# Kernel tuning notes

Measured on AMD Instinct MI355X. Metric: run time of the kernel, lower is better.

Reference implementation:

```python
import jax, jax.numpy as jnp
import numpy as np

C = 32          # mid_channel / in_channel
B = 8           # batch size (number of scenes)
N = 2_000_000   # total points across batch
BN_EPS = 1e-4   # BatchNorm1d eps from norm_fn


def setup_inputs() -> dict:
    key = jax.random.key(0)
    ks = jax.random.split(key, 8)
    s = 0.05
    return {
        "feats": jax.random.normal(ks[0], (N, C), dtype=jnp.float32),
        "batch_idxs": jnp.sort(jax.random.randint(ks[1], (N,), 0, B, dtype=jnp.int32)),
        "off_w1": jax.random.normal(ks[2], (C, C), dtype=jnp.float32) * s,
        "off_b1": jnp.zeros((C,), jnp.float32),
        "bn_gamma": jnp.ones((C,), jnp.float32),   # set_bn_init fills 1.0
        "bn_beta": jnp.zeros((C,), jnp.float32),   # set_bn_init fills 0.0
        "off_w2": jax.random.normal(ks[3], (C, 3), dtype=jnp.float32) * s,
        "off_b2": jnp.zeros((3,), jnp.float32),
        "mask_w1": jax.random.normal(ks[4], (C, C), dtype=jnp.float32) * s,
        "mask_b1": jnp.zeros((C,), jnp.float32),
        "mask_w2": jax.random.normal(ks[5], (C, 1), dtype=jnp.float32) * s,
        "mask_b2": jnp.zeros((1,), jnp.float32),
        "iou_w": jax.random.normal(ks[6], (C, 1), dtype=jnp.float32) * s,
        "iou_b": jnp.zeros((1,), jnp.float32),
    }


def reference(feats, batch_idxs, off_w1, off_b1, bn_gamma, bn_beta, off_w2, off_b2,
              mask_w1, mask_b1, mask_w2, mask_b2, iou_w, iou_b):
    # offset_linear = MLP([C, C, 3], norm_fn=BatchNorm1d): Linear -> BN -> ReLU -> Linear
    h = feats @ off_w1 + off_b1                      # [N, C]
    mu = h.mean(axis=0)
    var = jnp.mean(jnp.square(h - mu), axis=0)       # biased var (torch BN training fwd)
    h = (h - mu) * jax.lax.rsqrt(var + BN_EPS) * bn_gamma + bn_beta
    h = jax.nn.relu(h)
    pt_offsets = h @ off_w2 + off_b2                 # [N, 3]

    # mask_linear = MLP([C, C, 1], norm_fn=None): Linear -> ReLU -> Linear
    m = jax.nn.relu(feats @ mask_w1 + mask_b1)       # [N, C]
    mask_scores = m @ mask_w2 + mask_b2              # [N, 1]

    # global_pool: scatter mean of features over per-batch segments (batch offsets)
    ones = jnp.ones((feats.shape[0],), feats.dtype)
    counts = jax.ops.segment_sum(ones, batch_idxs, num_segments=B)          # [B]
    pooled = jax.ops.segment_sum(feats, batch_idxs, num_segments=B)         # [B, C]
    pooled = pooled / jnp.maximum(counts, 1.0)[:, None]

    # iou_score_linear on the pooled proposal feature
    iou_scores = pooled @ iou_w + iou_b              # [B, 1]
    return pt_offsets, mask_scores, pooled, iou_scores
```

## Files before the change

kernel.cpp:

```cpp
#include <hip/hip_runtime.h>

#define TPB 256

typedef __attribute__((ext_vector_type(8))) short short8;
typedef __attribute__((ext_vector_type(4))) float floatx4;

__device__ __forceinline__ unsigned short bf_trunc(float f){
    union { float f; unsigned u; } c; c.f = f;
    return (unsigned short)(c.u >> 16);
}
__device__ __forceinline__ unsigned short bf_rne(float f){
    union { float f; unsigned u; } c; c.f = f;
    unsigned r = c.u + 0x7fffu + ((c.u >> 16) & 1u);
    return (unsigned short)(r >> 16);
}

__global__ __launch_bounds__(TPB, 4) void pass1_kernel(
    const float* __restrict__ feats, const int* __restrict__ bidx,
    const float* __restrict__ w1, const float* __restrict__ b1,
    const float* __restrict__ mw1, const float* __restrict__ mb1,
    const float* __restrict__ mw2, const float* __restrict__ mb2,
    float* __restrict__ mask_out,
    float* __restrict__ ws_sum, float* __restrict__ ws_sq,
    float* __restrict__ ws_pool, int N)
{
    __shared__ float s_pool[8][32];
    __shared__ float s_sum[32];
    __shared__ float s_sq[32];

    const int tid  = threadIdx.x;
    const int lane = tid & 63;
    const int p = lane & 15;
    const int q = lane >> 4;

    if (tid < 32){ s_sum[tid] = 0.f; s_sq[tid] = 0.f; }
    ((float*)s_pool)[tid] = 0.f;
    __syncthreads();

    short8 aw0, aw1, am0, am1;
    floatx4 ci_h0, ci_h1, ci_m0, ci_m1;
    float mw2v[8];
#pragma unroll
    for (int j = 0; j < 8; ++j){
        const int k = q * 8 + j;
        aw0[j] = (short)bf_rne(w1 [k * 32 + p]);
        aw1[j] = (short)bf_rne(w1 [k * 32 + 16 + p]);
        am0[j] = (short)bf_rne(mw1[k * 32 + p]);
        am1[j] = (short)bf_rne(mw1[k * 32 + 16 + p]);
    }
#pragma unroll
    for (int r = 0; r < 4; ++r){
        const int c0 = q * 4 + r, c1 = 16 + q * 4 + r;
        ci_h0[r] = b1[c0];  ci_h1[r] = b1[c1];
        ci_m0[r] = mb1[c0]; ci_m1[r] = mb1[c1];
        mw2v[r] = mw2[c0];  mw2v[4 + r] = mw2[c1];
    }
    const float mb2s = mb2[0];

    float hsum[8] = {0,0,0,0,0,0,0,0};
    float hsq [8] = {0,0,0,0,0,0,0,0};
    float pacc[8] = {0,0,0,0,0,0,0,0};
    int curb = -1;

    const int  ntiles = (N + 15) >> 4;
    const long nw  = (long)gridDim.x * (TPB / 64);
    const long wid = (long)blockIdx.x * (TPB / 64) + (tid >> 6);
    const int  t0 = (int)(wid * (long)ntiles / nw);
    const int  t1 = (int)((wid + 1) * (long)ntiles / nw);

    floatx4 v0 = {0.f,0.f,0.f,0.f}, v1 = {0.f,0.f,0.f,0.f};
    int b = -1;
    if (t0 < t1){
        const int row = (t0 << 4) + p;
        if (row < N){
            const floatx4* rp = (const floatx4*)(feats + (size_t)row * 32 + q * 8);
            v0 = rp[0]; v1 = rp[1];
            b  = bidx[row];
        }
    }

    for (int t = t0; t < t1; ++t){
        floatx4 nv0 = {0.f,0.f,0.f,0.f}, nv1 = {0.f,0.f,0.f,0.f};
        int nb = -1;
        if (t + 1 < t1){
            const int nrow = ((t + 1) << 4) + p;
            if (nrow < N){
                const floatx4* rp = (const floatx4*)(feats + (size_t)nrow * 32 + q * 8);
                nv0 = rp[0]; nv1 = rp[1];
                nb  = bidx[nrow];
            }
        }

        const bool valid = (b >= 0);
        if (b != curb){
            if (curb >= 0){
#pragma unroll
                for (int j = 0; j < 8; ++j){
                    atomicAdd(&s_pool[curb][q * 8 + j], pacc[j]);
                    pacc[j] = 0.f;
                }
            }
            curb = b;
        }
        if (valid){
            pacc[0] += v0[0]; pacc[1] += v0[1]; pacc[2] += v0[2]; pacc[3] += v0[3];
            pacc[4] += v1[0]; pacc[5] += v1[1]; pacc[6] += v1[2]; pacc[7] += v1[3];
        }

        short8 bfrag;
        bfrag[0] = (short)bf_trunc(v0[0]); bfrag[1] = (short)bf_trunc(v0[1]);
        bfrag[2] = (short)bf_trunc(v0[2]); bfrag[3] = (short)bf_trunc(v0[3]);
        bfrag[4] = (short)bf_trunc(v1[0]); bfrag[5] = (short)bf_trunc(v1[1]);
        bfrag[6] = (short)bf_trunc(v1[2]); bfrag[7] = (short)bf_trunc(v1[3]);

        const floatx4 ch0 = __builtin_amdgcn_mfma_f32_16x16x32_bf16(aw0, bfrag, ci_h0, 0, 0, 0);
        const floatx4 ch1 = __builtin_amdgcn_mfma_f32_16x16x32_bf16(aw1, bfrag, ci_h1, 0, 0, 0);
        const floatx4 cm0 = __builtin_amdgcn_mfma_f32_16x16x32_bf16(am0, bfrag, ci_m0, 0, 0, 0);
        const floatx4 cm1 = __builtin_amdgcn_mfma_f32_16x16x32_bf16(am1, bfrag, ci_m1, 0, 0, 0);

        if (valid){
#pragma unroll
            for (int r = 0; r < 4; ++r){
                const float h0 = ch0[r]; hsum[r]     += h0; hsq[r]     = fmaf(h0, h0, hsq[r]);
                const float h1 = ch1[r]; hsum[4 + r] += h1; hsq[4 + r] = fmaf(h1, h1, hsq[4 + r]);
            }
        }

        float tm = 0.f;
#pragma unroll
        for (int r = 0; r < 4; ++r){
            tm = fmaf(fmaxf(cm0[r], 0.f), mw2v[r],     tm);
            tm = fmaf(fmaxf(cm1[r], 0.f), mw2v[4 + r], tm);
        }
        tm += __shfl_xor(tm, 16, 64);
        tm += __shfl_xor(tm, 32, 64);
        if (q == 0 && valid) mask_out[(t << 4) + p] = tm + mb2s;

        v0 = nv0; v1 = nv1; b = nb;
    }

    if (curb >= 0){
#pragma unroll
        for (int j = 0; j < 8; ++j) atomicAdd(&s_pool[curb][q * 8 + j], pacc[j]);
    }
#pragma unroll
    for (int i = 0; i < 8; ++i){
        const int ch = (i >> 2) * 16 + q * 4 + (i & 3);
        atomicAdd(&s_sum[ch], hsum[i]);
        atomicAdd(&s_sq[ch],  hsq[i]);
    }
    __syncthreads();
    if (tid < 32){
        atomicAdd(&ws_sum[tid], s_sum[tid]);
        atomicAdd(&ws_sq[tid],  s_sq[tid]);
    }
    {
        const float pv = ((float*)s_pool)[tid];
        if (pv != 0.f) atomicAdd(&ws_pool[tid], pv);
    }
}

__global__ __launch_bounds__(TPB, 4) void pass2_kernel(
    const float* __restrict__ feats, const int* __restrict__ bidx,
    const float* __restrict__ w1, const float* __restrict__ b1,
    const float* __restrict__ gamma, const float* __restrict__ beta,
    const float* __restrict__ w2, const float* __restrict__ b2,
    const float* __restrict__ iw, const float* __restrict__ ib,
    const float* __restrict__ ws_sum, const float* __restrict__ ws_sq,
    const float* __restrict__ ws_pool,
    float* __restrict__ pt_out, float* __restrict__ pooled_out,
    float* __restrict__ iou_out, int N, int B)
{
    __shared__ float s_sc[32];
    __shared__ float s_bp[32];
    __shared__ float s_pooled[256];
    __shared__ int   s_lb[33];

    const int tid  = threadIdx.x;
    const int lane = tid & 63;
    const int p = lane & 15;
    const int q = lane >> 4;

    if (tid < 32){
        const float invN = 1.f / (float)N;
        const float mu  = ws_sum[tid] * invN;
        const float var = ws_sq[tid] * invN - mu * mu;
        const float s   = gamma[tid] * rsqrtf(var + 1e-4f);
        s_sc[tid] = s;
        s_bp[tid] = (b1[tid] - mu) * s + beta[tid];
    }
    __syncthreads();

    if (blockIdx.x == 0){
        if (tid <= B){
            int lo = 0, hi = N;
            while (lo < hi){
                const int mid = (lo + hi) >> 1;
                if (bidx[mid] < tid) lo = mid + 1; else hi = mid;
            }
            s_lb[tid] = lo;
        }
        __syncthreads();
        if (tid < B * 32){
            const int bb = tid >> 5;
            const float cnt = fmaxf((float)(s_lb[bb + 1] - s_lb[bb]), 1.f);
            const float pv = ws_pool[tid] / cnt;
            s_pooled[tid]   = pv;
            pooled_out[tid] = pv;
        }
        __syncthreads();
        if (tid < B){
            float acc = ib[0];
#pragma unroll
            for (int i = 0; i < 32; ++i) acc = fmaf(s_pooled[tid * 32 + i], iw[i], acc);
            iou_out[tid] = acc;
        }
    }

    short8 pw0, pw1;
    floatx4 pc0, pc1;
    float w2v[24];
    const float sc0 = s_sc[p], sc1 = s_sc[16 + p];
#pragma unroll
    for (int j = 0; j < 8; ++j){
        const int k = q * 8 + j;
        pw0[j] = (short)bf_rne(w1[k * 32 + p]      * sc0);
        pw1[j] = (short)bf_rne(w1[k * 32 + 16 + p] * sc1);
    }
#pragma unroll
    for (int r = 0; r < 4; ++r){
        pc0[r] = s_bp[q * 4 + r];
        pc1[r] = s_bp[16 + q * 4 + r];
    }
#pragma unroll
    for (int i = 0; i < 8; ++i){
        const int ch = (i >> 2) * 16 + q * 4 + (i & 3);
        w2v[i]      = w2[ch * 3 + 0];
        w2v[8 + i]  = w2[ch * 3 + 1];
        w2v[16 + i] = w2[ch * 3 + 2];
    }
    const float b2v0 = b2[0], b2v1 = b2[1], b2v2 = b2[2];

    const int  ntiles = (N + 15) >> 4;
    const long nw  = (long)gridDim.x * (TPB / 64);
    const long wid = (long)blockIdx.x * (TPB / 64) + (tid >> 6);
    const int  t0 = (int)(wid * (long)ntiles / nw);
    const int  t1 = (int)((wid + 1) * (long)ntiles / nw);

    floatx4 v0 = {0.f,0.f,0.f,0.f}, v1 = {0.f,0.f,0.f,0.f};
    bool valid = false;
    if (t0 < t1){
        const int row = (t0 << 4) + p;
        if (row < N){
            const floatx4* rp = (const floatx4*)(feats + (size_t)row * 32 + q * 8);
            v0 = rp[0]; v1 = rp[1];
            valid = true;
        }
    }

    for (int t = t0; t < t1; ++t){
        floatx4 nv0 = {0.f,0.f,0.f,0.f}, nv1 = {0.f,0.f,0.f,0.f};
        bool nvalid = false;
        if (t + 1 < t1){
            const int nrow = ((t + 1) << 4) + p;
            if (nrow < N){
                const floatx4* rp = (const floatx4*)(feats + (size_t)nrow * 32 + q * 8);
                nv0 = rp[0]; nv1 = rp[1];
                nvalid = true;
            }
        }

        short8 bfrag;
        bfrag[0] = (short)bf_trunc(v0[0]); bfrag[1] = (short)bf_trunc(v0[1]);
        bfrag[2] = (short)bf_trunc(v0[2]); bfrag[3] = (short)bf_trunc(v0[3]);
        bfrag[4] = (short)bf_trunc(v1[0]); bfrag[5] = (short)bf_trunc(v1[1]);
        bfrag[6] = (short)bf_trunc(v1[2]); bfrag[7] = (short)bf_trunc(v1[3]);

        const floatx4 c0 = __builtin_amdgcn_mfma_f32_16x16x32_bf16(pw0, bfrag, pc0, 0, 0, 0);
        const floatx4 c1 = __builtin_amdgcn_mfma_f32_16x16x32_bf16(pw1, bfrag, pc1, 0, 0, 0);

        float s0 = 0.f, s1 = 0.f, s2 = 0.f;
#pragma unroll
        for (int r = 0; r < 4; ++r){
            const float p0 = fmaxf(c0[r], 0.f);
            const float p1 = fmaxf(c1[r], 0.f);
            s0 = fmaf(p0, w2v[r],      s0); s0 = fmaf(p1, w2v[4 + r],  s0);
            s1 = fmaf(p0, w2v[8 + r],  s1); s1 = fmaf(p1, w2v[12 + r], s1);
            s2 = fmaf(p0, w2v[16 + r], s2); s2 = fmaf(p1, w2v[20 + r], s2);
        }
        s0 += __shfl_xor(s0, 16, 64); s0 += __shfl_xor(s0, 32, 64);
        s1 += __shfl_xor(s1, 16, 64); s1 += __shfl_xor(s1, 32, 64);
        s2 += __shfl_xor(s2, 16, 64); s2 += __shfl_xor(s2, 32, 64);

        if (lane < 48 && valid){
            float val = (q == 0) ? (s0 + b2v0) : ((q == 1) ? (s1 + b2v1) : (s2 + b2v2));
            pt_out[(size_t)(t << 4) * 3 + p * 3 + q] = val;
        }

        v0 = nv0; v1 = nv1; valid = nvalid;
    }
}

extern "C" void kernel_launch(void* const* d_in, const int* in_sizes, int n_in,
                              void* d_out, int out_size, void* d_ws, size_t ws_size,
                              hipStream_t stream) {
    const float* feats = (const float*)d_in[0];
    const int*   bidx  = (const int*)d_in[1];
    const float* w1    = (const float*)d_in[2];
    const float* b1    = (const float*)d_in[3];
    const float* gamma = (const float*)d_in[4];
    const float* beta  = (const float*)d_in[5];
    const float* w2    = (const float*)d_in[6];
    const float* b2    = (const float*)d_in[7];
    const float* mw1   = (const float*)d_in[8];
    const float* mb1   = (const float*)d_in[9];
    const float* mw2   = (const float*)d_in[10];
    const float* mb2   = (const float*)d_in[11];
    const float* iw    = (const float*)d_in[12];
    const float* ib    = (const float*)d_in[13];

    const int N = in_sizes[0] / 32;
    const int B = (out_size - 4 * N) / 33;

    float* out    = (float*)d_out;
    float* pt     = out;
    float* mask   = out + (size_t)3 * N;
    float* pooled = out + (size_t)4 * N;
    float* iou    = pooled + (size_t)B * 32;

    float* ws      = (float*)d_ws;
    float* ws_sum  = ws;
    float* ws_sq   = ws + 32;
    float* ws_pool = ws + 64;

    hipMemsetAsync(ws, 0, (size_t)(64 + B * 32) * sizeof(float), stream);

    int dev = 0;
    hipGetDevice(&dev);
    hipDeviceProp_t prop;
    hipGetDeviceProperties(&prop, dev);
    int per1 = 0, per2 = 0;
    hipOccupancyMaxActiveBlocksPerMultiprocessor(&per1, pass1_kernel, TPB, 0);
    hipOccupancyMaxActiveBlocksPerMultiprocessor(&per2, pass2_kernel, TPB, 0);
    int g1 = per1 * prop.multiProcessorCount; if (g1 < 256) g1 = 256;
    int g2 = per2 * prop.multiProcessorCount; if (g2 < 256) g2 = 256;

    pass1_kernel<<<g1, TPB, 0, stream>>>(feats, bidx, w1, b1, mw1, mb1, mw2, mb2,
                                         mask, ws_sum, ws_sq, ws_pool, N);
    pass2_kernel<<<g2, TPB, 0, stream>>>(feats, bidx, w1, b1, gamma, beta, w2, b2,
                                         iw, ib, ws_sum, ws_sq, ws_pool,
                                         pt, pooled, iou, N, B);
}
```

Baseline: 438.8 us.

## Grid-stride tiles, binary-search segment bounds, and perm-based bf16 packing

Both passes now walk 16-row tiles in a grid-stride order instead of giving each wave one contiguous chunk, so concurrently active waves read adjacent memory. Pass1 no longer loads batch_idxs per row. Each block binary-searches the segment boundaries once into shared memory and uses a fast path for tiles that lie inside one segment, with a per-row slow path only at boundary tiles. The bf16 conversion uses a byte-perm to pack two truncated values per instruction. This relies on batch_idxs being sorted, and the extra boundary crossings per wave add some more LDS atomics.

Result: slower. 468.0 us (+6.6%).

```diff
diff --git a/kernel.cpp b/kernel.cpp
--- a/kernel.cpp
+++ b/kernel.cpp
@@ -13,6 +13,10 @@
     union { float f; unsigned u; } c; c.f = f;
     unsigned r = c.u + 0x7fffu + ((c.u >> 16) & 1u);
     return (unsigned short)(r >> 16);
+}
+__device__ __forceinline__ unsigned pack_bf(float lo, float hi){
+    union { float f; unsigned u; } a, b; a.f = lo; b.f = hi;
+    return __builtin_amdgcn_perm(b.u, a.u, 0x07060302u);
 }
 
 __global__ __launch_bounds__(TPB, 4) void pass1_kernel(
@@ -22,11 +26,12 @@
     const float* __restrict__ mw2, const float* __restrict__ mb2,
     float* __restrict__ mask_out,
     float* __restrict__ ws_sum, float* __restrict__ ws_sq,
-    float* __restrict__ ws_pool, int N)
+    float* __restrict__ ws_pool, int N, int B)
 {
     __shared__ float s_pool[8][32];
     __shared__ float s_sum[32];
     __shared__ float s_sq[32];
+    __shared__ int   s_lb[9];
 
     const int tid  = threadIdx.x;
     const int lane = tid & 63;
@@ -35,6 +40,14 @@
 
     if (tid < 32){ s_sum[tid] = 0.f; s_sq[tid] = 0.f; }
     ((float*)s_pool)[tid] = 0.f;
+    if (tid <= B){
+        int lo = 0, hi = N;
+        while (lo < hi){
+            const int mid = (lo + hi) >> 1;
+            if (bidx[mid] < tid) lo = mid + 1; else hi = mid;
+        }
+        s_lb[tid] = lo;
+    }
     __syncthreads();
 
     short8 aw0, aw1, am0, am1;
@@ -60,70 +73,96 @@
     float hsum[8] = {0,0,0,0,0,0,0,0};
     float hsq [8] = {0,0,0,0,0,0,0,0};
     float pacc[8] = {0,0,0,0,0,0,0,0};
-    int curb = -1;
-
-    const int  ntiles = (N + 15) >> 4;
-    const long nw  = (long)gridDim.x * (TPB / 64);
-    const long wid = (long)blockIdx.x * (TPB / 64) + (tid >> 6);
-    const int  t0 = (int)(wid * (long)ntiles / nw);
-    const int  t1 = (int)((wid + 1) * (long)ntiles / nw);
+
+    const int ntiles = (N + 15) >> 4;
+    const int nw  = gridDim.x * (TPB / 64);
+    const int wid = blockIdx.x * (TPB / 64) + (tid >> 6);
+
+    int curb = 0;
+    {
+        const int r0 = wid << 4;
+        while (curb < B - 1 && r0 >= s_lb[curb + 1]) curb++;
+    }
+    int lbn = s_lb[curb + 1];
+
+    const size_t dstep = ((size_t)nw) << 9;
+    const float* rp = feats + (((size_t)wid) << 9) + (p << 5) + (q << 3);
 
     floatx4 v0 = {0.f,0.f,0.f,0.f}, v1 = {0.f,0.f,0.f,0.f};
-    int b = -1;
-    if (t0 < t1){
-        const int row = (t0 << 4) + p;
-        if (row < N){
-            const floatx4* rp = (const floatx4*)(feats + (size_t)row * 32 + q * 8);
-            v0 = rp[0]; v1 = rp[1];
-            b  = bidx[row];
-        }
-    }
-
-    for (int t = t0; t < t1; ++t){
+    if (wid < ntiles){
+        if (((wid << 4) + p) < N){
+            const floatx4* vp = (const floatx4*)rp;
+            v0 = vp[0]; v1 = vp[1];
+        }
+    }
+
+    for (int t = wid; t < ntiles; t += nw){
         floatx4 nv0 = {0.f,0.f,0.f,0.f}, nv1 = {0.f,0.f,0.f,0.f};
-        int nb = -1;
-        if (t + 1 < t1){
-            const int nrow = ((t + 1) << 4) + p;
-            if (nrow < N){
-                const floatx4* rp = (const floatx4*)(feats + (size_t)nrow * 32 + q * 8);
-                nv0 = rp[0]; nv1 = rp[1];
-                nb  = bidx[nrow];
-            }
-        }
-
-        const bool valid = (b >= 0);
-        if (b != curb){
-            if (curb >= 0){
-#pragma unroll
-                for (int j = 0; j < 8; ++j){
-                    atomicAdd(&s_pool[curb][q * 8 + j], pacc[j]);
-                    pacc[j] = 0.f;
-                }
-            }
-            curb = b;
-        }
-        if (valid){
+        const float* np = rp + dstep;
+        if (t + nw < ntiles){
+            if ((((t + nw) << 4) + p) < N){
+                const floatx4* vp = (const floatx4*)np;
+                nv0 = vp[0]; nv1 = vp[1];
+            }
+        }
+
+        const int r0 = t << 4;
+        if (r0 >= lbn){
+#pragma unroll
+            for (int j = 0; j < 8; ++j){
+                if (pacc[j] != 0.f) atomicAdd(&s_pool[curb][q * 8 + j], pacc[j]);
+                pacc[j] = 0.f;
+            }
+            do { curb++; } while (curb < B - 1 && r0 >= s_lb[curb + 1]);
+            lbn = s_lb[curb + 1];
+        }
+        const bool slow = (r0 + 15 >= lbn);
+
+        if (!slow){
             pacc[0] += v0[0]; pacc[1] += v0[1]; pacc[2] += v0[2]; pacc[3] += v0[3];
             pacc[4] += v1[0]; pacc[5] += v1[1]; pacc[6] += v1[2]; pacc[7] += v1[3];
+        } else {
+            const int row = r0 + p;
+            if (row < N){
+                int bl = curb;
+                for (int c = curb + 1; c < B; ++c) bl += (row >= s_lb[c]);
+                atomicAdd(&s_pool[bl][q * 8 + 0], v0[0]);
+                atomicAdd(&s_pool[bl][q * 8 + 1], v0[1]);
+                atomicAdd(&s_pool[bl][q * 8 + 2], v0[2]);
+                atomicAdd(&s_pool[bl][q * 8 + 3], v0[3]);
+                atomicAdd(&s_pool[bl][q * 8 + 4], v1[0]);
+                atomicAdd(&s_pool[bl][q * 8 + 5], v1[1]);
+                atomicAdd(&s_pool[bl][q * 8 + 6], v1[2]);
+                atomicAdd(&s_pool[bl][q * 8 + 7], v1[3]);
+            }
         }
 
         short8 bfrag;
-        bfrag[0] = (short)bf_trunc(v0[0]); bfrag[1] = (short)bf_trunc(v0[1]);
-        bfrag[2] = (short)bf_trunc(v0[2]); bfrag[3] = (short)bf_trunc(v0[3]);
-        bfrag[4] = (short)bf_trunc(v1[0]); bfrag[5] = (short)bf_trunc(v1[1]);
-        bfrag[6] = (short)bf_trunc(v1[2]); bfrag[7] = (short)bf_trunc(v1[3]);
+        {
+            unsigned* bw = (unsigned*)&bfrag;
+            bw[0] = pack_bf(v0[0], v0[1]);
+            bw[1] = pack_bf(v0[2], v0[3]);
+            bw[2] = pack_bf(v1[0], v1[1]);
+            bw[3] = pack_bf(v1[2], v1[3]);
+        }
 
         const floatx4 ch0 = __builtin_amdgcn_mfma_f32_16x16x32_bf16(aw0, bfrag, ci_h0, 0, 0, 0);
         const floatx4 ch1 = __builtin_amdgcn_mfma_f32_16x16x32_bf16(aw1, bfrag, ci_h1, 0, 0, 0);
         const floatx4 cm0 = __builtin_amdgcn_mfma_f32_16x16x32_bf16(am0, bfrag, ci_m0, 0, 0, 0);
         const floatx4 cm1 = __builtin_amdgcn_mfma_f32_16x16x32_bf16(am1, bfrag, ci_m1, 0, 0, 0);
 
-        if (valid){
+        if (!slow){
 #pragma unroll
             for (int r = 0; r < 4; ++r){
                 const float h0 = ch0[r]; hsum[r]     += h0; hsq[r]     = fmaf(h0, h0, hsq[r]);
                 const float h1 = ch1[r]; hsum[4 + r] += h1; hsq[4 + r] = fmaf(h1, h1, hsq[4 + r]);
             }
+        } else if (r0 + p < N){
+#pragma unroll
+            for (int r = 0; r < 4; ++r){
+                const float h0 = ch0[r]; hsum[r]     += h0; hsq[r]     = fmaf(h0, h0, hsq[r]);
+                const float h1 = ch1[r]; hsum[4 + r] += h1; hsq[4 + r] = fmaf(h1, h1, hsq[4 + r]);
+            }
         }
 
         float tm = 0.f;
@@ -134,14 +173,14 @@
         }
         tm += __shfl_xor(tm, 16, 64);
         tm += __shfl_xor(tm, 32, 64);
-        if (q == 0 && valid) mask_out[(t << 4) + p] = tm + mb2s;
-
-        v0 = nv0; v1 = nv1; b = nb;
-    }
-
-    if (curb >= 0){
-#pragma unroll
-        for (int j = 0; j < 8; ++j) atomicAdd(&s_pool[curb][q * 8 + j], pacc[j]);
+        if (q == 0 && (r0 + p) < N) mask_out[r0 + p] = tm + mb2s;
+
+        v0 = nv0; v1 = nv1; rp = np;
+    }
+
+#pragma unroll
+    for (int j = 0; j < 8; ++j){
+        if (pacc[j] != 0.f) atomicAdd(&s_pool[curb][q * 8 + j], pacc[j]);
     }
 #pragma unroll
     for (int i = 0; i < 8; ++i){
@@ -241,40 +280,39 @@
     }
     const float b2v0 = b2[0], b2v1 = b2[1], b2v2 = b2[2];
 
-    const int  ntiles = (N + 15) >> 4;
-    const long nw  = (long)gridDim.x * (TPB / 64);
-    const long wid = (long)blockIdx.x * (TPB / 64) + (tid >> 6);
-    const int  t0 = (int)(wid * (long)ntiles / nw);
-    const int  t1 = (int)((wid + 1) * (long)ntiles / nw);
+    const int ntiles = (N + 15) >> 4;
+    const int nw  = gridDim.x * (TPB / 64);
+    const int wid = blockIdx.x * (TPB / 64) + (tid >> 6);
+
+    const size_t dstep = ((size_t)nw) << 9;
+    const float* rp = feats + (((size_t)wid) << 9) + (p << 5) + (q << 3);
 
     floatx4 v0 = {0.f,0.f,0.f,0.f}, v1 = {0.f,0.f,0.f,0.f};
-    bool valid = false;
-    if (t0 < t1){
-        const int row = (t0 << 4) + p;
-        if (row < N){
-            const floatx4* rp = (const floatx4*)(feats + (size_t)row * 32 + q * 8);
-            v0 = rp[0]; v1 = rp[1];
-            valid = true;
-        }
-    }
-
-    for (int t = t0; t < t1; ++t){
+    if (wid < ntiles){
+        if (((wid << 4) + p) < N){
+            const floatx4* vp = (const floatx4*)rp;
+            v0 = vp[0]; v1 = vp[1];
+        }
+    }
+
+    for (int t = wid; t < ntiles; t += nw){
         floatx4 nv0 = {0.f,0.f,0.f,0.f}, nv1 = {0.f,0.f,0.f,0.f};
-        bool nvalid = false;
-        if (t + 1 < t1){
-            const int nrow = ((t + 1) << 4) + p;
-            if (nrow < N){
-                const floatx4* rp = (const floatx4*)(feats + (size_t)nrow * 32 + q * 8);
-                nv0 = rp[0]; nv1 = rp[1];
-                nvalid = true;
+        const float* np = rp + dstep;
+        if (t + nw < ntiles){
+            if ((((t + nw) << 4) + p) < N){
+                const floatx4* vp = (const floatx4*)np;
+                nv0 = vp[0]; nv1 = vp[1];
             }
         }
 
         short8 bfrag;
-        bfrag[0] = (short)bf_trunc(v0[0]); bfrag[1] = (short)bf_trunc(v0[1]);
-        bfrag[2] = (short)bf_trunc(v0[2]); bfrag[3] = (short)bf_trunc(v0[3]);
-        bfrag[4] = (short)bf_trunc(v1[0]); bfrag[5] = (short)bf_trunc(v1[1]);
-        bfrag[6] = (short)bf_trunc(v1[2]); bfrag[7] = (short)bf_trunc(v1[3]);
+        {
+            unsigned* bw = (unsigned*)&bfrag;
+            bw[0] = pack_bf(v0[0], v0[1]);
+            bw[1] = pack_bf(v0[2], v0[3]);
+            bw[2] = pack_bf(v1[0], v1[1]);
+            bw[3] = pack_bf(v1[2], v1[3]);
+        }
 
         const floatx4 c0 = __builtin_amdgcn_mfma_f32_16x16x32_bf16(pw0, bfrag, pc0, 0, 0, 0);
         const floatx4 c1 = __builtin_amdgcn_mfma_f32_16x16x32_bf16(pw1, bfrag, pc1, 0, 0, 0);
@@ -292,12 +330,13 @@
         s1 += __shfl_xor(s1, 16, 64); s1 += __shfl_xor(s1, 32, 64);
         s2 += __shfl_xor(s2, 16, 64); s2 += __shfl_xor(s2, 32, 64);
 
-        if (lane < 48 && valid){
+        const int row = (t << 4) + p;
+        if (lane < 48 && row < N){
             float val = (q == 0) ? (s0 + b2v0) : ((q == 1) ? (s1 + b2v1) : (s2 + b2v2));
             pt_out[(size_t)(t << 4) * 3 + p * 3 + q] = val;
         }
 
-        v0 = nv0; v1 = nv1; valid = nvalid;
+        v0 = nv0; v1 = nv1; rp = np;
     }
 }
 
@@ -346,7 +385,7 @@
     int g2 = per2 * prop.multiProcessorCount; if (g2 < 256) g2 = 256;
 
     pass1_kernel<<<g1, TPB, 0, stream>>>(feats, bidx, w1, b1, mw1, mb1, mw2, mb2,
-                                         mask, ws_sum, ws_sq, ws_pool, N);
+                                         mask, ws_sum, ws_sq, ws_pool, N, B);
     pass2_kernel<<<g2, TPB, 0, stream>>>(feats, bidx, w1, b1, gamma, beta, w2, b2,
                                          iw, ib, ws_sum, ws_sq, ws_pool,
                                          pt, pooled, iou, N, B);
```
